# Optimization experiments

Hardware: AMD Instinct MI355X
Metric: run time of the kernel (lower is better)

Reference implementation:

```python
import jax, jax.numpy as jnp
import numpy as np

B, K, SD, NA = 2, 512, 60, 5
E, H, D, FF, NL = 256, 4, 64, 1024, 2
EPS_F = 1e-6   # feature_eps in phi(x)=relu(x)+eps
LN_EPS = 1e-5  # torch LayerNorm default eps


def setup_inputs() -> dict:
    key = jax.random.key(0)
    ks = jax.random.split(key, 16)
    f = lambda i, shape, s=0.02: jax.random.normal(ks[i], shape, dtype=jnp.float32) * s
    return {
        "rtg": jax.random.normal(ks[0], (B, K, 1), dtype=jnp.float32),
        "state": jax.random.normal(ks[1], (B, K, SD), dtype=jnp.float32),
        "action": jax.random.normal(ks[2], (B, K, NA), dtype=jnp.float32),
        "rtg_w": f(3, (1, E)), "rtg_b": jnp.zeros((E,), jnp.float32),
        "state_w": f(4, (SD, E)), "state_b": jnp.zeros((E,), jnp.float32),
        "action_w": f(5, (NA, E)), "action_b": jnp.zeros((E,), jnp.float32),
        "pos_emb": f(6, (K, E)),
        "norm1_g": jnp.ones((NL, E), jnp.float32), "norm1_b": jnp.zeros((NL, E), jnp.float32),
        "qkv_w": f(7, (NL, E, 3 * E)), "qkv_b": jnp.zeros((NL, 3 * E), jnp.float32),
        "out_w": f(8, (NL, E, E)), "out_b": jnp.zeros((NL, E), jnp.float32),
        "norm2_g": jnp.ones((NL, E), jnp.float32), "norm2_b": jnp.zeros((NL, E), jnp.float32),
        "ffn1_w": f(9, (NL, E, FF)), "ffn1_b": jnp.zeros((NL, FF), jnp.float32),
        "ffn2_w": f(10, (NL, FF, E)), "ffn2_b": jnp.zeros((NL, E), jnp.float32),
        "normf_g": jnp.ones((E,), jnp.float32), "normf_b": jnp.zeros((E,), jnp.float32),
        "pred_w": f(11, (E, NA)), "pred_b": jnp.zeros((NA,), jnp.float32),
    }


def _ln(x, g, b):
    m = x.mean(-1, keepdims=True)
    v = jnp.mean((x - m) ** 2, -1, keepdims=True)
    return (x - m) * jax.lax.rsqrt(v + LN_EPS) * g + b


def _attn(x, qkv_w, qkv_b, out_w, out_b):
    b, l, _ = x.shape
    qkv = (x @ qkv_w + qkv_b).reshape(b, l, 3, H, D).transpose(2, 0, 3, 1, 4)
    q, k, v = qkv[0], qkv[1], qkv[2]          # each (b,h,l,d)
    q = jax.nn.relu(q) + EPS_F
    k = jax.nn.relu(k) + EPS_F
    kv = jnp.cumsum(jnp.einsum('bhld,bhle->bhlde', k, v), axis=2)  # (b,h,l,d,e)
    kcum = jnp.cumsum(k, axis=2)
    num = jnp.einsum('bhld,bhlde->bhle', q, kv)
    den = jnp.maximum(jnp.einsum('bhld,bhld->bhl', q, kcum)[..., None], 1e-6)
    o = (num / den).transpose(0, 2, 1, 3).reshape(b, l, H * D)
    return o @ out_w + out_b


def reference(rtg, state, action, rtg_w, rtg_b, state_w, state_b, action_w, action_b,
              pos_emb, norm1_g, norm1_b, qkv_w, qkv_b, out_w, out_b,
              norm2_g, norm2_b, ffn1_w, ffn1_b, ffn2_w, ffn2_b,
              normf_g, normf_b, pred_w, pred_b):
    b, k, _ = state.shape
    p = pos_emb[:k][None]
    r = rtg @ rtg_w + rtg_b + p
    s = state @ state_w + state_b + p
    a = action @ action_w + action_b + p
    # interleave (r,s,a) per timestep -> (b, 3k, E)
    x = jnp.stack((r, s, a), axis=2).reshape(b, 3 * k, E)
    for i in range(NL):
        x = x + _attn(_ln(x, norm1_g[i], norm1_b[i]), qkv_w[i], qkv_b[i], out_w[i], out_b[i])
        h = _ln(x, norm2_g[i], norm2_b[i])
        h = jax.nn.gelu(h @ ffn1_w[i] + ffn1_b[i], approximate=False) @ ffn2_w[i] + ffn2_b[i]
        x = x + h
    x = _ln(x, normf_g, normf_b)
    return x[:, 1::3, :] @ pred_w + pred_b  # predict from state tokens -> (b,k,num_actions)
```

## Files before the change

### kernel.cpp

```cpp
#include <hip/hip_runtime.h>
#include <hip/hip_bf16.h>
#include <math.h>

#define B_  2
#define K_  512
#define SD_ 60
#define NA_ 5
#define E_  256
#define H_  4
#define D_  64
#define FF_ 1024
#define NL_ 2
#define L_  (3 * K_)
#define M_  (B_ * L_)
#define EPS_F 1e-6f
#define LN_EPS 1e-5f
#define CHK 64
#define NC_ (L_ / CHK)

using bf16x8 = __attribute__((ext_vector_type(8))) short;
using f32x4  = __attribute__((ext_vector_type(4))) float;
typedef unsigned short u16;

__device__ inline u16 f2b(float v) {
    __hip_bfloat16 h = __float2bfloat16(v);
    return *(u16*)&h;
}
__device__ inline float b2f(u16 v) {
    __hip_bfloat16 h = *(__hip_bfloat16*)&v;
    return __bfloat162float(h);
}

__global__ __launch_bounds__(256) void init_kernel(
    const float* __restrict__ qkv_w, const float* __restrict__ out_w,
    const float* __restrict__ ffn1_w, const float* __restrict__ ffn2_w,
    u16* __restrict__ qkvT, u16* __restrict__ outT,
    u16* __restrict__ f1T, u16* __restrict__ f2T,
    const float* __restrict__ rtg, const float* __restrict__ state,
    const float* __restrict__ action,
    const float* __restrict__ rtg_w, const float* __restrict__ rtg_b,
    const float* __restrict__ state_w, const float* __restrict__ state_b,
    const float* __restrict__ action_w, const float* __restrict__ action_b,
    const float* __restrict__ pos,
    const float* __restrict__ g, const float* __restrict__ bta,
    float* __restrict__ X, u16* __restrict__ Y)
{
    __shared__ u16 T[32][33];
    if (blockIdx.x < 1536) {
        int tb = blockIdx.x;
        int layer = tb / 768;
        int r = tb % 768;
        const float* src; u16* dst; int K, N, tidx;
        if (r < 192)      { src = qkv_w  + layer * 196608; dst = qkvT + layer * 196608; K = 256;  N = 768;  tidx = r; }
        else if (r < 256) { src = out_w  + layer * 65536;  dst = outT + layer * 65536;  K = 256;  N = 256;  tidx = r - 192; }
        else if (r < 512) { src = ffn1_w + layer * 262144; dst = f1T  + layer * 262144; K = 256;  N = 1024; tidx = r - 256; }
        else              { src = ffn2_w + layer * 262144; dst = f2T  + layer * 262144; K = 1024; N = 256;  tidx = r - 512; }
        int tilesN = N >> 5;
        int k0 = (tidx / tilesN) << 5;
        int n0 = (tidx % tilesN) << 5;
        int c = threadIdx.x & 31, r0 = threadIdx.x >> 5;
        for (int rr = r0; rr < 32; rr += 8)
            T[rr][c] = f2b(src[(size_t)(k0 + rr) * N + n0 + c]);
        __syncthreads();
        for (int rr = r0; rr < 32; rr += 8)
            dst[(size_t)(n0 + rr) * K + k0 + c] = T[c][rr];
        return;
    }
    int tok = (blockIdx.x - 1536) * 4 + (threadIdx.x >> 6);
    int lane = threadIdx.x & 63;
    int b = tok / L_, l = tok % L_;
    int j = l % 3, t = l / 3;
    int e0 = lane * 4;
    float4 val = *(const float4*)(pos + t * E_ + e0);
    if (j == 0) {
        float rv = rtg[b * K_ + t];
        float4 w = *(const float4*)(rtg_w + e0);
        float4 bb = *(const float4*)(rtg_b + e0);
        val.x += rv * w.x + bb.x; val.y += rv * w.y + bb.y;
        val.z += rv * w.z + bb.z; val.w += rv * w.w + bb.w;
    } else if (j == 1) {
        float4 a = *(const float4*)(state_b + e0);
        const float* srow = state + ((size_t)b * K_ + t) * SD_;
        for (int i = 0; i < SD_; i++) {
            float s = srow[i];
            float4 w = *(const float4*)(state_w + (size_t)i * E_ + e0);
            a.x += s * w.x; a.y += s * w.y; a.z += s * w.z; a.w += s * w.w;
        }
        val.x += a.x; val.y += a.y; val.z += a.z; val.w += a.w;
    } else {
        float4 a = *(const float4*)(action_b + e0);
        const float* arow = action + ((size_t)b * K_ + t) * NA_;
        #pragma unroll
        for (int i = 0; i < NA_; i++) {
            float s = arow[i];
            float4 w = *(const float4*)(action_w + (size_t)i * E_ + e0);
            a.x += s * w.x; a.y += s * w.y; a.z += s * w.z; a.w += s * w.w;
        }
        val.x += a.x; val.y += a.y; val.z += a.z; val.w += a.w;
    }
    *(float4*)(X + (size_t)tok * E_ + e0) = val;
    float s = val.x + val.y + val.z + val.w;
    #pragma unroll
    for (int o = 32; o; o >>= 1) s += __shfl_xor(s, o, 64);
    float mean = s * (1.f / E_);
    float dx = val.x - mean, dy = val.y - mean, dz = val.z - mean, dw = val.w - mean;
    float q = dx * dx + dy * dy + dz * dz + dw * dw;
    #pragma unroll
    for (int o = 32; o; o >>= 1) q += __shfl_xor(q, o, 64);
    float inv = rsqrtf(q * (1.f / E_) + LN_EPS);
    float4 gv = *(const float4*)(g + e0);
    float4 bv = *(const float4*)(bta + e0);
    ushort4 u;
    u.x = f2b(dx * inv * gv.x + bv.x); u.y = f2b(dy * inv * gv.y + bv.y);
    u.z = f2b(dz * inv * gv.z + bv.z); u.w = f2b(dw * inv * gv.w + bv.w);
    *(ushort4*)(Y + (size_t)tok * E_ + e0) = u;
}

__global__ __launch_bounds__(256) void ln_kernel(
    const float* __restrict__ X, const float* __restrict__ g,
    const float* __restrict__ b, u16* __restrict__ Y)
{
    int tok = blockIdx.x * 4 + (threadIdx.x >> 6);
    int lane = threadIdx.x & 63;
    int e0 = lane * 4;
    float4 v = *(const float4*)(X + (size_t)tok * E_ + e0);
    float s = v.x + v.y + v.z + v.w;
    #pragma unroll
    for (int o = 32; o; o >>= 1) s += __shfl_xor(s, o, 64);
    float mean = s * (1.f / E_);
    float dx = v.x - mean, dy = v.y - mean, dz = v.z - mean, dw = v.w - mean;
    float q = dx * dx + dy * dy + dz * dz + dw * dw;
    #pragma unroll
    for (int o = 32; o; o >>= 1) q += __shfl_xor(q, o, 64);
    float inv = rsqrtf(q * (1.f / E_) + LN_EPS);
    float4 gv = *(const float4*)(g + e0);
    float4 bv = *(const float4*)(b + e0);
    ushort4 u;
    u.x = f2b(dx * inv * gv.x + bv.x); u.y = f2b(dy * inv * gv.y + bv.y);
    u.z = f2b(dz * inv * gv.z + bv.z); u.w = f2b(dw * inv * gv.w + bv.w);
    *(ushort4*)(Y + (size_t)tok * E_ + e0) = u;
}

template <int EPI>
__global__ __launch_bounds__(256) void mgemm(
    const u16* __restrict__ A, const u16* __restrict__ Bt,
    const float* __restrict__ bias,
    u16* __restrict__ C, int M, int N, int Kd)
{
    __shared__ __align__(16) u16 As[128 * 40];
    __shared__ __align__(16) u16 Bs[128 * 40];
    int tid = threadIdx.x;
    int bm = blockIdx.y * 128, bn = blockIdx.x * 128;
    int wave = tid >> 6, lane = tid & 63;
    int wm = (wave >> 1) * 64, wn = (wave & 1) * 64;
    int lr = lane & 15, kg = lane >> 4;

    int r0 = tid >> 2, g0 = (tid & 3) * 8;
    int r1 = (tid + 256) >> 2, g1 = (tid & 3) * 8;

    f32x4 acc[4][4] = {};

    for (int k0 = 0; k0 < Kd; k0 += 32) {
        uint4 a0 = *(const uint4*)(A + (size_t)(bm + r0) * Kd + k0 + g0);
        uint4 a1 = *(const uint4*)(A + (size_t)(bm + r1) * Kd + k0 + g1);
        uint4 b0 = *(const uint4*)(Bt + (size_t)(bn + r0) * Kd + k0 + g0);
        uint4 b1 = *(const uint4*)(Bt + (size_t)(bn + r1) * Kd + k0 + g1);
        __syncthreads();
        *(uint4*)&As[r0 * 40 + g0] = a0;
        *(uint4*)&As[r1 * 40 + g1] = a1;
        *(uint4*)&Bs[r0 * 40 + g0] = b0;
        *(uint4*)&Bs[r1 * 40 + g1] = b1;
        __syncthreads();
        bf16x8 af[4], bg[4];
        #pragma unroll
        for (int i = 0; i < 4; i++)
            af[i] = *(const bf16x8*)&As[(wm + i * 16 + lr) * 40 + kg * 8];
        #pragma unroll
        for (int j = 0; j < 4; j++)
            bg[j] = *(const bf16x8*)&Bs[(wn + j * 16 + lr) * 40 + kg * 8];
        #pragma unroll
        for (int i = 0; i < 4; i++)
            #pragma unroll
            for (int j = 0; j < 4; j++)
                acc[i][j] = __builtin_amdgcn_mfma_f32_16x16x32_bf16(
                    af[i], bg[j], acc[i][j], 0, 0, 0);
    }

    #pragma unroll
    for (int i = 0; i < 4; i++) {
        #pragma unroll
        for (int j = 0; j < 4; j++) {
            int col = bn + wn + j * 16 + lr;
            float bc = bias[col];
            #pragma unroll
            for (int r = 0; r < 4; r++) {
                int row = bm + wm + i * 16 + kg * 4 + r;
                float v = acc[i][j][r] + bc;
                if (EPI == 1) v = 0.5f * v * (1.0f + erff(v * 0.70710678118654752f));
                C[(size_t)row * N + col] = f2b(v);
            }
        }
    }
}

__global__ __launch_bounds__(256) void gemm64res(
    const u16* __restrict__ A, const u16* __restrict__ Bt,
    const float* __restrict__ bias, float* __restrict__ X, int Kd)
{
    __shared__ __align__(16) u16 As[64 * 40];
    __shared__ __align__(16) u16 Bs[64 * 40];
    int tid = threadIdx.x;
    int tile = blockIdx.x;
    int bm = (tile >> 2) * 64, bn = (tile & 3) * 64;
    int wave = tid >> 6, lane = tid & 63;
    int wm = (wave >> 1) * 32, wn = (wave & 1) * 32;
    int lr = lane & 15, kg = lane >> 4;
    int r = tid >> 2, g = (tid & 3) * 8;

    f32x4 acc[2][2] = {};
    for (int k0 = 0; k0 < Kd; k0 += 32) {
        uint4 a0 = *(const uint4*)(A + (size_t)(bm + r) * Kd + k0 + g);
        uint4 b0 = *(const uint4*)(Bt + (size_t)(bn + r) * Kd + k0 + g);
        __syncthreads();
        *(uint4*)&As[r * 40 + g] = a0;
        *(uint4*)&Bs[r * 40 + g] = b0;
        __syncthreads();
        bf16x8 af[2], bg[2];
        #pragma unroll
        for (int i = 0; i < 2; i++)
            af[i] = *(const bf16x8*)&As[(wm + i * 16 + lr) * 40 + kg * 8];
        #pragma unroll
        for (int j = 0; j < 2; j++)
            bg[j] = *(const bf16x8*)&Bs[(wn + j * 16 + lr) * 40 + kg * 8];
        #pragma unroll
        for (int i = 0; i < 2; i++)
            #pragma unroll
            for (int j = 0; j < 2; j++)
                acc[i][j] = __builtin_amdgcn_mfma_f32_16x16x32_bf16(
                    af[i], bg[j], acc[i][j], 0, 0, 0);
    }
    #pragma unroll
    for (int i = 0; i < 2; i++) {
        #pragma unroll
        for (int j = 0; j < 2; j++) {
            int col = bn + wn + j * 16 + lr;
            float bc = bias[col];
            #pragma unroll
            for (int rr = 0; rr < 4; rr++) {
                int row = bm + wm + i * 16 + kg * 4 + rr;
                float v = acc[i][j][rr] + bc + X[(size_t)row * 256 + col];
                X[(size_t)row * 256 + col] = v;
            }
        }
    }
}

__global__ __launch_bounds__(256) void chunk_sum_kernel(
    const u16* __restrict__ QKV, float* __restrict__ S, float* __restrict__ Z)
{
    int blk = blockIdx.x;
    int c = blk % NC_;
    int bh = blk / NC_;
    int h = bh % H_;
    int b = bh / H_;
    __shared__ __align__(16) u16 Kt[64 * 72];
    __shared__ __align__(16) u16 Vt[64 * 72];
    int tid = threadIdx.x;
    const size_t base = ((size_t)b * L_ + (size_t)c * CHK) * 768 + h * 64;
    for (int i = tid; i < 1024; i += 256) {
        int t = i >> 4, d4 = (i & 15) << 2;
        ushort4 k = *(const ushort4*)(QKV + base + (size_t)t * 768 + 256 + d4);
        ushort4 v = *(const ushort4*)(QKV + base + (size_t)t * 768 + 512 + d4);
        Kt[(d4 + 0) * 72 + t] = f2b(fmaxf(b2f(k.x), 0.f) + EPS_F);
        Kt[(d4 + 1) * 72 + t] = f2b(fmaxf(b2f(k.y), 0.f) + EPS_F);
        Kt[(d4 + 2) * 72 + t] = f2b(fmaxf(b2f(k.z), 0.f) + EPS_F);
        Kt[(d4 + 3) * 72 + t] = f2b(fmaxf(b2f(k.w), 0.f) + EPS_F);
        Vt[(d4 + 0) * 72 + t] = v.x;
        Vt[(d4 + 1) * 72 + t] = v.y;
        Vt[(d4 + 2) * 72 + t] = v.z;
        Vt[(d4 + 3) * 72 + t] = v.w;
    }
    __syncthreads();
    int wave = tid >> 6, lane = tid & 63;
    int lr = lane & 15, kg = lane >> 4;
    int wm = wave * 16;
    bf16x8 a0 = *(const bf16x8*)&Kt[(wm + lr) * 72 + kg * 8];
    bf16x8 a1 = *(const bf16x8*)&Kt[(wm + lr) * 72 + 32 + kg * 8];
    f32x4 acc[4] = {};
    #pragma unroll
    for (int j = 0; j < 4; j++) {
        bf16x8 b0 = *(const bf16x8*)&Vt[(j * 16 + lr) * 72 + kg * 8];
        bf16x8 b1 = *(const bf16x8*)&Vt[(j * 16 + lr) * 72 + 32 + kg * 8];
        acc[j] = __builtin_amdgcn_mfma_f32_16x16x32_bf16(a0, b0, acc[j], 0, 0, 0);
        acc[j] = __builtin_amdgcn_mfma_f32_16x16x32_bf16(a1, b1, acc[j], 0, 0, 0);
    }
    if (tid < 64) {
        float z = 0.f;
        #pragma unroll 8
        for (int t = 0; t < 64; t++) z += b2f(Kt[tid * 72 + t]);
        Z[(size_t)blk * 64 + tid] = z;
    }
    float* Sp = S + (size_t)blk * 4096;
    #pragma unroll
    for (int j = 0; j < 4; j++) {
        #pragma unroll
        for (int rr = 0; rr < 4; rr++) {
            int d = wm + kg * 4 + rr;
            int e = j * 16 + lr;
            Sp[d * 64 + e] = acc[j][rr];
        }
    }
}

__global__ __launch_bounds__(256) void chunk_out_kernel(
    const u16* __restrict__ QKV, const float* __restrict__ S,
    const float* __restrict__ Z, u16* __restrict__ O)
{
    int blk = blockIdx.x;
    int c = blk % NC_;
    int bh = blk / NC_;
    int h = bh % H_;
    int b = bh / H_;
    __shared__ __align__(16) u16 Qb[64 * 72];
    __shared__ __align__(16) u16 Kb[64 * 72];
    __shared__ __align__(16) u16 Vt[64 * 72];
    __shared__ __align__(16) u16 KVt[64 * 72];
    __shared__ __align__(16) u16 Ps[64 * 72];
    __shared__ float kzs[64];
    __shared__ float rows[64];
    __shared__ float invs[64];
    int tid = threadIdx.x;
    const size_t base = ((size_t)b * L_ + (size_t)c * CHK) * 768 + h * 64;
    const float* Sbh = S + (size_t)bh * NC_ * 4096;
    for (int i = tid; i < 1024; i += 256) {
        int t = i >> 4, d4 = (i & 15) << 2;
        ushort4 q = *(const ushort4*)(QKV + base + (size_t)t * 768 + d4);
        ushort4 k = *(const ushort4*)(QKV + base + (size_t)t * 768 + 256 + d4);
        ushort4 v = *(const ushort4*)(QKV + base + (size_t)t * 768 + 512 + d4);
        ushort4 qu, ku;
        qu.x = f2b(fmaxf(b2f(q.x), 0.f) + EPS_F); qu.y = f2b(fmaxf(b2f(q.y), 0.f) + EPS_F);
        qu.z = f2b(fmaxf(b2f(q.z), 0.f) + EPS_F); qu.w = f2b(fmaxf(b2f(q.w), 0.f) + EPS_F);
        ku.x = f2b(fmaxf(b2f(k.x), 0.f) + EPS_F); ku.y = f2b(fmaxf(b2f(k.y), 0.f) + EPS_F);
        ku.z = f2b(fmaxf(b2f(k.z), 0.f) + EPS_F); ku.w = f2b(fmaxf(b2f(k.w), 0.f) + EPS_F);
        *(ushort4*)&Qb[t * 72 + d4] = qu;
        *(ushort4*)&Kb[t * 72 + d4] = ku;
        Vt[(d4 + 0) * 72 + t] = v.x;
        Vt[(d4 + 1) * 72 + t] = v.y;
        Vt[(d4 + 2) * 72 + t] = v.z;
        Vt[(d4 + 3) * 72 + t] = v.w;
        int d = t, e4 = d4;
        float4 a = make_float4(0.f, 0.f, 0.f, 0.f);
        for (int cc = 0; cc < c; cc++) {
            float4 s4 = *(const float4*)(Sbh + (size_t)cc * 4096 + d * 64 + e4);
            a.x += s4.x; a.y += s4.y; a.z += s4.z; a.w += s4.w;
        }
        KVt[(e4 + 0) * 72 + d] = f2b(a.x);
        KVt[(e4 + 1) * 72 + d] = f2b(a.y);
        KVt[(e4 + 2) * 72 + d] = f2b(a.z);
        KVt[(e4 + 3) * 72 + d] = f2b(a.w);
    }
    if (tid < 64) {
        float z = 0.f;
        const float* Zbh = Z + (size_t)bh * NC_ * 64;
        for (int cc = 0; cc < c; cc++) z += Zbh[cc * 64 + tid];
        kzs[tid] = z;
    }
    __syncthreads();

    int wave = tid >> 6, lane = tid & 63;
    int lr = lane & 15, kg = lane >> 4;
    int wm = wave * 16;

    bf16x8 aq0 = *(const bf16x8*)&Qb[(wm + lr) * 72 + kg * 8];
    bf16x8 aq1 = *(const bf16x8*)&Qb[(wm + lr) * 72 + 32 + kg * 8];

    f32x4 accs[4] = {};
    #pragma unroll
    for (int j = 0; j < 4; j++) {
        bf16x8 b0 = *(const bf16x8*)&Kb[(j * 16 + lr) * 72 + kg * 8];
        bf16x8 b1 = *(const bf16x8*)&Kb[(j * 16 + lr) * 72 + 32 + kg * 8];
        accs[j] = __builtin_amdgcn_mfma_f32_16x16x32_bf16(aq0, b0, accs[j], 0, 0, 0);
        accs[j] = __builtin_amdgcn_mfma_f32_16x16x32_bf16(aq1, b1, accs[j], 0, 0, 0);
    }
    float rsum[4] = {0.f, 0.f, 0.f, 0.f};
    #pragma unroll
    for (int j = 0; j < 4; j++) {
        #pragma unroll
        for (int rr = 0; rr < 4; rr++) {
            int m = wm + kg * 4 + rr;
            int n = j * 16 + lr;
            float v = (n <= m) ? accs[j][rr] : 0.f;
            rsum[rr] += v;
            Ps[m * 72 + n] = f2b(v);
        }
    }
    #pragma unroll
    for (int rr = 0; rr < 4; rr++) {
        float s = rsum[rr];
        s += __shfl_xor(s, 1, 64);
        s += __shfl_xor(s, 2, 64);
        s += __shfl_xor(s, 4, 64);
        s += __shfl_xor(s, 8, 64);
        if (lr == 0) rows[wm + kg * 4 + rr] = s;
    }
    __syncthreads();

    if (tid < 64) {
        float den = rows[tid];
        float acc = 0.f;
        #pragma unroll 8
        for (int d = 0; d < 64; d++) acc += b2f(Qb[tid * 72 + d]) * kzs[d];
        invs[tid] = 1.f / fmaxf(den + acc, 1e-6f);
    }

    bf16x8 ap0 = *(const bf16x8*)&Ps[(wm + lr) * 72 + kg * 8];
    bf16x8 ap1 = *(const bf16x8*)&Ps[(wm + lr) * 72 + 32 + kg * 8];
    f32x4 accn[4] = {};
    #pragma unroll
    for (int j = 0; j < 4; j++) {
        bf16x8 b0 = *(const bf16x8*)&KVt[(j * 16 + lr) * 72 + kg * 8];
        bf16x8 b1 = *(const bf16x8*)&KVt[(j * 16 + lr) * 72 + 32 + kg * 8];
        accn[j] = __builtin_amdgcn_mfma_f32_16x16x32_bf16(aq0, b0, accn[j], 0, 0, 0);
        accn[j] = __builtin_amdgcn_mfma_f32_16x16x32_bf16(aq1, b1, accn[j], 0, 0, 0);
        bf16x8 c0 = *(const bf16x8*)&Vt[(j * 16 + lr) * 72 + kg * 8];
        bf16x8 c1 = *(const bf16x8*)&Vt[(j * 16 + lr) * 72 + 32 + kg * 8];
        accn[j] = __builtin_amdgcn_mfma_f32_16x16x32_bf16(ap0, c0, accn[j], 0, 0, 0);
        accn[j] = __builtin_amdgcn_mfma_f32_16x16x32_bf16(ap1, c1, accn[j], 0, 0, 0);
    }
    __syncthreads();

    u16* Op = O + ((size_t)b * L_ + (size_t)c * CHK) * E_ + h * 64;
    #pragma unroll
    for (int j = 0; j < 4; j++) {
        #pragma unroll
        for (int rr = 0; rr < 4; rr++) {
            int m = wm + kg * 4 + rr;
            int e = j * 16 + lr;
            Op[(size_t)m * E_ + e] = f2b(accn[j][rr] * invs[m]);
        }
    }
}

__global__ __launch_bounds__(256) void lnpred_kernel(
    const float* __restrict__ X, const float* __restrict__ g,
    const float* __restrict__ bt, const float* __restrict__ W,
    const float* __restrict__ bias, float* __restrict__ Out)
{
    int si = blockIdx.x * 4 + (threadIdx.x >> 6);
    int lane = threadIdx.x & 63;
    int b = si / K_, t = si % K_;
    size_t row = (size_t)b * L_ + 3 * t + 1;
    int e0 = lane * 4;
    float4 v = *(const float4*)(X + row * E_ + e0);
    float s = v.x + v.y + v.z + v.w;
    #pragma unroll
    for (int o = 32; o; o >>= 1) s += __shfl_xor(s, o, 64);
    float mean = s * (1.f / E_);
    float dx = v.x - mean, dy = v.y - mean, dz = v.z - mean, dw = v.w - mean;
    float q = dx * dx + dy * dy + dz * dz + dw * dw;
    #pragma unroll
    for (int o = 32; o; o >>= 1) q += __shfl_xor(q, o, 64);
    float inv = rsqrtf(q * (1.f / E_) + LN_EPS);
    float4 gv = *(const float4*)(g + e0);
    float4 bv = *(const float4*)(bt + e0);
    float y0 = dx * inv * gv.x + bv.x;
    float y1 = dy * inv * gv.y + bv.y;
    float y2 = dz * inv * gv.z + bv.z;
    float y3 = dw * inv * gv.w + bv.w;
    #pragma unroll
    for (int na = 0; na < NA_; na++) {
        float a = y0 * W[(e0 + 0) * NA_ + na] + y1 * W[(e0 + 1) * NA_ + na]
                + y2 * W[(e0 + 2) * NA_ + na] + y3 * W[(e0 + 3) * NA_ + na];
        #pragma unroll
        for (int o = 32; o; o >>= 1) a += __shfl_xor(a, o, 64);
        if (lane == 0) Out[(size_t)si * NA_ + na] = a + bias[na];
    }
}

extern "C" void kernel_launch(void* const* d_in, const int* in_sizes, int n_in,
                              void* d_out, int out_size, void* d_ws, size_t ws_size,
                              hipStream_t stream) {
    const float* rtg      = (const float*)d_in[0];
    const float* state    = (const float*)d_in[1];
    const float* action   = (const float*)d_in[2];
    const float* rtg_w    = (const float*)d_in[3];
    const float* rtg_b    = (const float*)d_in[4];
    const float* state_w  = (const float*)d_in[5];
    const float* state_b  = (const float*)d_in[6];
    const float* action_w = (const float*)d_in[7];
    const float* action_b = (const float*)d_in[8];
    const float* pos_emb  = (const float*)d_in[9];
    const float* norm1_g  = (const float*)d_in[10];
    const float* norm1_b  = (const float*)d_in[11];
    const float* qkv_w    = (const float*)d_in[12];
    const float* qkv_b    = (const float*)d_in[13];
    const float* out_w    = (const float*)d_in[14];
    const float* out_b    = (const float*)d_in[15];
    const float* norm2_g  = (const float*)d_in[16];
    const float* norm2_b  = (const float*)d_in[17];
    const float* ffn1_w   = (const float*)d_in[18];
    const float* ffn1_b   = (const float*)d_in[19];
    const float* ffn2_w   = (const float*)d_in[20];
    const float* ffn2_b   = (const float*)d_in[21];
    const float* normf_g  = (const float*)d_in[22];
    const float* normf_b  = (const float*)d_in[23];
    const float* pred_w   = (const float*)d_in[24];
    const float* pred_b   = (const float*)d_in[25];
    float* out = (float*)d_out;

    float* ws = (float*)d_ws;
    float* x    = ws;
    float* S    = x + 786432;
    float* Z    = S + 786432;
    u16*   yb   = (u16*)(Z + 12288);
    u16*   qkvb = yb + 786432;
    u16*   att  = qkvb + 2359296;
    u16*   h1   = att + 786432;
    u16*   qkvT = h1 + 3145728;
    u16*   outT = qkvT + 393216;
    u16*   f1T  = outT + 131072;
    u16*   f2T  = f1T + 524288;

    init_kernel<<<2304, 256, 0, stream>>>(
        qkv_w, out_w, ffn1_w, ffn2_w, qkvT, outT, f1T, f2T,
        rtg, state, action, rtg_w, rtg_b, state_w, state_b,
        action_w, action_b, pos_emb, norm1_g, norm1_b, x, yb);

    for (int i = 0; i < NL_; i++) {
        mgemm<0><<<dim3(768 / 128, M_ / 128), 256, 0, stream>>>(
            yb, qkvT + (size_t)i * 196608, qkv_b + i * 768, qkvb,
            M_, 768, E_);
        chunk_sum_kernel<<<B_ * H_ * NC_, 256, 0, stream>>>(qkvb, S, Z);
        chunk_out_kernel<<<B_ * H_ * NC_, 256, 0, stream>>>(qkvb, S, Z, att);
        gemm64res<<<M_ / 64 * 4, 256, 0, stream>>>(
            att, outT + (size_t)i * 65536, out_b + i * E_, x, E_);
        ln_kernel<<<M_ / 4, 256, 0, stream>>>(
            x, norm2_g + i * E_, norm2_b + i * E_, yb);
        mgemm<1><<<dim3(FF_ / 128, M_ / 128), 256, 0, stream>>>(
            yb, f1T + (size_t)i * 262144, ffn1_b + i * FF_, h1,
            M_, FF_, E_);
        gemm64res<<<M_ / 64 * 4, 256, 0, stream>>>(
            h1, f2T + (size_t)i * 262144, ffn2_b + i * E_, x, FF_);
        if (i == 0)
            ln_kernel<<<M_ / 4, 256, 0, stream>>>(
                x, norm1_g + E_, norm1_b + E_, yb);
    }
    lnpred_kernel<<<(B_ * K_) / 4, 256, 0, stream>>>(
        x, normf_g, normf_b, pred_w, pred_b, out);
}
```

Before: 277.5 us.

## Double-buffer LDS tiles in GEMM kernels and widen residual GEMM K-step

Both bf16 MFMA GEMM kernels now use two shared-memory buffers. The next K tile is loaded into registers before the current tile's MFMAs run, then written to the other buffer, which needs only one barrier per iteration. The residual GEMM also raises its K step from 32 to 64 (two MFMAs per fragment pair) with a padded 72-element row stride. This hides global-load latency and halves barrier count, at the cost of double the LDS use and more registers, which can lower occupancy.

```diff
diff --git a/kernel.cpp b/kernel.cpp
--- a/kernel.cpp
+++ b/kernel.cpp
@@ -147,8 +147,8 @@
     const float* __restrict__ bias,
     u16* __restrict__ C, int M, int N, int Kd)
 {
-    __shared__ __align__(16) u16 As[128 * 40];
-    __shared__ __align__(16) u16 Bs[128 * 40];
+    __shared__ __align__(16) u16 As[2][128 * 40];
+    __shared__ __align__(16) u16 Bs[2][128 * 40];
     int tid = threadIdx.x;
     int bm = blockIdx.y * 128, bn = blockIdx.x * 128;
     int wave = tid >> 6, lane = tid & 63;
@@ -156,34 +156,53 @@
     int lr = lane & 15, kg = lane >> 4;
 
     int r0 = tid >> 2, g0 = (tid & 3) * 8;
-    int r1 = (tid + 256) >> 2, g1 = (tid & 3) * 8;
+    int r1 = r0 + 64;
+
+    const u16* Ap0 = A + (size_t)(bm + r0) * Kd + g0;
+    const u16* Ap1 = A + (size_t)(bm + r1) * Kd + g0;
+    const u16* Bp0 = Bt + (size_t)(bn + r0) * Kd + g0;
+    const u16* Bp1 = Bt + (size_t)(bn + r1) * Kd + g0;
+
+    uint4 a0 = *(const uint4*)(Ap0);
+    uint4 a1 = *(const uint4*)(Ap1);
+    uint4 b0 = *(const uint4*)(Bp0);
+    uint4 b1 = *(const uint4*)(Bp1);
+    *(uint4*)&As[0][r0 * 40 + g0] = a0;
+    *(uint4*)&As[0][r1 * 40 + g0] = a1;
+    *(uint4*)&Bs[0][r0 * 40 + g0] = b0;
+    *(uint4*)&Bs[0][r1 * 40 + g0] = b1;
 
     f32x4 acc[4][4] = {};
-
-    for (int k0 = 0; k0 < Kd; k0 += 32) {
-        uint4 a0 = *(const uint4*)(A + (size_t)(bm + r0) * Kd + k0 + g0);
-        uint4 a1 = *(const uint4*)(A + (size_t)(bm + r1) * Kd + k0 + g1);
-        uint4 b0 = *(const uint4*)(Bt + (size_t)(bn + r0) * Kd + k0 + g0);
-        uint4 b1 = *(const uint4*)(Bt + (size_t)(bn + r1) * Kd + k0 + g1);
+    int NT = Kd >> 5;
+    for (int t = 0; t < NT; ++t) {
+        int cur = t & 1;
         __syncthreads();
-        *(uint4*)&As[r0 * 40 + g0] = a0;
-        *(uint4*)&As[r1 * 40 + g1] = a1;
-        *(uint4*)&Bs[r0 * 40 + g0] = b0;
-        *(uint4*)&Bs[r1 * 40 + g1] = b1;
-        __syncthreads();
+        if (t + 1 < NT) {
+            int k1 = (t + 1) << 5;
+            a0 = *(const uint4*)(Ap0 + k1);
+            a1 = *(const uint4*)(Ap1 + k1);
+            b0 = *(const uint4*)(Bp0 + k1);
+            b1 = *(const uint4*)(Bp1 + k1);
+        }
         bf16x8 af[4], bg[4];
         #pragma unroll
         for (int i = 0; i < 4; i++)
-            af[i] = *(const bf16x8*)&As[(wm + i * 16 + lr) * 40 + kg * 8];
+            af[i] = *(const bf16x8*)&As[cur][(wm + i * 16 + lr) * 40 + kg * 8];
         #pragma unroll
         for (int j = 0; j < 4; j++)
-            bg[j] = *(const bf16x8*)&Bs[(wn + j * 16 + lr) * 40 + kg * 8];
+            bg[j] = *(const bf16x8*)&Bs[cur][(wn + j * 16 + lr) * 40 + kg * 8];
         #pragma unroll
         for (int i = 0; i < 4; i++)
             #pragma unroll
             for (int j = 0; j < 4; j++)
                 acc[i][j] = __builtin_amdgcn_mfma_f32_16x16x32_bf16(
                     af[i], bg[j], acc[i][j], 0, 0, 0);
+        if (t + 1 < NT) {
+            *(uint4*)&As[cur ^ 1][r0 * 40 + g0] = a0;
+            *(uint4*)&As[cur ^ 1][r1 * 40 + g0] = a1;
+            *(uint4*)&Bs[cur ^ 1][r0 * 40 + g0] = b0;
+            *(uint4*)&Bs[cur ^ 1][r1 * 40 + g0] = b1;
+        }
     }
 
     #pragma unroll
@@ -207,37 +226,66 @@
     const u16* __restrict__ A, const u16* __restrict__ Bt,
     const float* __restrict__ bias, float* __restrict__ X, int Kd)
 {
-    __shared__ __align__(16) u16 As[64 * 40];
-    __shared__ __align__(16) u16 Bs[64 * 40];
+    __shared__ __align__(16) u16 As[2][64 * 72];
+    __shared__ __align__(16) u16 Bs[2][64 * 72];
     int tid = threadIdx.x;
     int tile = blockIdx.x;
     int bm = (tile >> 2) * 64, bn = (tile & 3) * 64;
     int wave = tid >> 6, lane = tid & 63;
     int wm = (wave >> 1) * 32, wn = (wave & 1) * 32;
     int lr = lane & 15, kg = lane >> 4;
-    int r = tid >> 2, g = (tid & 3) * 8;
+    int r = tid >> 2, c8 = (tid & 3) * 8;
+
+    const u16* Ap = A + (size_t)(bm + r) * Kd + c8;
+    const u16* Bp = Bt + (size_t)(bn + r) * Kd + c8;
+
+    uint4 a0 = *(const uint4*)(Ap);
+    uint4 a1 = *(const uint4*)(Ap + 32);
+    uint4 b0 = *(const uint4*)(Bp);
+    uint4 b1 = *(const uint4*)(Bp + 32);
+    *(uint4*)&As[0][r * 72 + c8]      = a0;
+    *(uint4*)&As[0][r * 72 + 32 + c8] = a1;
+    *(uint4*)&Bs[0][r * 72 + c8]      = b0;
+    *(uint4*)&Bs[0][r * 72 + 32 + c8] = b1;
 
     f32x4 acc[2][2] = {};
-    for (int k0 = 0; k0 < Kd; k0 += 32) {
-        uint4 a0 = *(const uint4*)(A + (size_t)(bm + r) * Kd + k0 + g);
-        uint4 b0 = *(const uint4*)(Bt + (size_t)(bn + r) * Kd + k0 + g);
+    int NT = Kd >> 6;
+    for (int t = 0; t < NT; ++t) {
+        int cur = t & 1;
         __syncthreads();
-        *(uint4*)&As[r * 40 + g] = a0;
-        *(uint4*)&Bs[r * 40 + g] = b0;
-        __syncthreads();
-        bf16x8 af[2], bg[2];
-        #pragma unroll
-        for (int i = 0; i < 2; i++)
-            af[i] = *(const bf16x8*)&As[(wm + i * 16 + lr) * 40 + kg * 8];
-        #pragma unroll
-        for (int j = 0; j < 2; j++)
-            bg[j] = *(const bf16x8*)&Bs[(wn + j * 16 + lr) * 40 + kg * 8];
+        if (t + 1 < NT) {
+            int k1 = (t + 1) << 6;
+            a0 = *(const uint4*)(Ap + k1);
+            a1 = *(const uint4*)(Ap + k1 + 32);
+            b0 = *(const uint4*)(Bp + k1);
+            b1 = *(const uint4*)(Bp + k1 + 32);
+        }
+        bf16x8 af0[2], af1[2], bg0[2], bg1[2];
+        #pragma unroll
+        for (int i = 0; i < 2; i++) {
+            af0[i] = *(const bf16x8*)&As[cur][(wm + i * 16 + lr) * 72 + kg * 8];
+            af1[i] = *(const bf16x8*)&As[cur][(wm + i * 16 + lr) * 72 + 32 + kg * 8];
+        }
+        #pragma unroll
+        for (int j = 0; j < 2; j++) {
+            bg0[j] = *(const bf16x8*)&Bs[cur][(wn + j * 16 + lr) * 72 + kg * 8];
+            bg1[j] = *(const bf16x8*)&Bs[cur][(wn + j * 16 + lr) * 72 + 32 + kg * 8];
+        }
         #pragma unroll
         for (int i = 0; i < 2; i++)
             #pragma unroll
-            for (int j = 0; j < 2; j++)
+            for (int j = 0; j < 2; j++) {
                 acc[i][j] = __builtin_amdgcn_mfma_f32_16x16x32_bf16(
-                    af[i], bg[j], acc[i][j], 0, 0, 0);
+                    af0[i], bg0[j], acc[i][j], 0, 0, 0);
+                acc[i][j] = __builtin_amdgcn_mfma_f32_16x16x32_bf16(
+                    af1[i], bg1[j], acc[i][j], 0, 0, 0);
+            }
+        if (t + 1 < NT) {
+            *(uint4*)&As[cur ^ 1][r * 72 + c8]      = a0;
+            *(uint4*)&As[cur ^ 1][r * 72 + 32 + c8] = a1;
+            *(uint4*)&Bs[cur ^ 1][r * 72 + c8]      = b0;
+            *(uint4*)&Bs[cur ^ 1][r * 72 + 32 + c8] = b1;
+        }
     }
     #pragma unroll
     for (int i = 0; i < 2; i++) {
```

After: 259.2 us. 6.6% less time.
